# Kernel tuning notes

Hardware: AMD Instinct MI355X
Metric: run time of the kernel (lower is better)

Reference implementation:

```python
import jax, jax.numpy as jnp
import numpy as np

B, N, D = 4, 9216, 512
NH, L = 8, 64            # num_heads, num_landmarks
HD = D // NH             # head_dim = 64
MLP = 4 * D              # mlp_ratio 4.0


def setup_inputs() -> dict:
    key = jax.random.key(0)
    ks = jax.random.split(key, 32)
    w = lambda k, shape: jax.random.normal(k, shape, jnp.float32) * 0.02
    return {
        'x': jax.random.normal(ks[0], (B, N, D), jnp.float32),
        # PPEG depthwise convs (groups=dim -> kernel (D,1,kh,kw))
        'conv1_w': w(ks[1], (D, 1, 3, 3)), 'conv1_b': w(ks[2], (D,)),
        'conv2_w': w(ks[3], (D, 1, 5, 5)), 'conv2_b': w(ks[4], (D,)),
        'conv3_w': w(ks[5], (D, 1, 7, 7)), 'conv3_b': w(ks[6], (D,)),
        'ppeg_g': jnp.ones((D,), jnp.float32), 'ppeg_b': jnp.zeros((D,), jnp.float32),
        'norm1_g': jnp.ones((D,), jnp.float32), 'norm1_b': jnp.zeros((D,), jnp.float32),
        'norm2_g': jnp.ones((D,), jnp.float32), 'norm2_b': jnp.zeros((D,), jnp.float32),
        # Nystrom attention projections (torch Linear: y = x @ W.T + b)
        'qkv_w': w(ks[7], (3 * D, D)), 'qkv_b': w(ks[8], (3 * D,)),
        'proj_w': w(ks[9], (D, D)), 'proj_b': w(ks[10], (D,)),
        # MLP
        'mlp_w1': w(ks[11], (MLP, D)), 'mlp_b1': w(ks[12], (MLP,)),
        'mlp_w2': w(ks[13], (D, MLP)), 'mlp_b2': w(ks[14], (D,)),
    }


def _layernorm(x, g, b):
    m = jnp.mean(x, axis=-1, keepdims=True)
    v = jnp.mean(jnp.square(x - m), axis=-1, keepdims=True)
    return (x - m) * jax.lax.rsqrt(v + 1e-5) * g + b


def _dwconv(x2d, w, b, pad):
    # x2d: (B, D, H, W); depthwise conv, groups = D
    y = jax.lax.conv_general_dilated(
        x2d, w, window_strides=(1, 1), padding=((pad, pad), (pad, pad)),
        feature_group_count=w.shape[0],
        dimension_numbers=('NCHW', 'OIHW', 'NCHW'))
    return y + b[None, :, None, None]


def _forward(x, conv1_w, conv1_b, conv2_w, conv2_b, conv3_w, conv3_b,
             ppeg_g, ppeg_b, norm1_g, norm1_b, norm2_g, norm2_b,
             qkv_w, qkv_b, proj_w, proj_b, mlp_w1, mlp_b1, mlp_w2, mlp_b2):
    Bx, Nx, Dx = x.shape
    # ---- PPEG ----
    H = int(np.sqrt(Nx)); W = (Nx + H - 1) // H
    x2d = x.reshape(Bx, H, W, Dx).transpose(0, 3, 1, 2)  # b d h w
    pos = (_dwconv(x2d, conv1_w, conv1_b, 1)
           + _dwconv(x2d, conv2_w, conv2_b, 2)
           + _dwconv(x2d, conv3_w, conv3_b, 3))
    pos = pos.transpose(0, 2, 3, 1).reshape(Bx, Nx, Dx)
    x = _layernorm(x + pos, ppeg_g, ppeg_b)
    # ---- Nystrom attention ----
    xn = _layernorm(x, norm1_g, norm1_b)
    qkv = xn @ qkv_w.T + qkv_b                      # (B, N, 3D)
    qkv = qkv.reshape(Bx, Nx, 3, NH, HD).transpose(2, 0, 3, 1, 4)
    q, k, v = qkv[0], qkv[1], qkv[2]                # (B, H, N, hd)
    scale = HD ** -0.5
    idx = np.linspace(0, Nx - 1, L).astype(np.int64)  # landmark indices (static)
    kl, ql = k[:, :, idx], q[:, :, idx]             # (B, H, L, hd)
    k1 = jax.nn.softmax(jnp.einsum('bhnd,bhld->bhnl', q, kl) * scale, axis=-1)
    k2 = jax.nn.softmax(jnp.einsum('bhld,bhmd->bhlm', ql, kl) * scale, axis=-1)
    k3 = jax.nn.softmax(jnp.einsum('bhld,bhnd->bhln', ql, k) * scale, axis=-1)
    k2_inv = jnp.linalg.pinv(k2 + 1e-6 * jnp.eye(L, dtype=x.dtype))
    # (k1 @ k2_inv @ k3) @ v, right-associated to avoid the NxN intermediate
    out = k1 @ (k2_inv @ (k3 @ v))                  # (B, H, N, hd)
    out = out.transpose(0, 2, 1, 3).reshape(Bx, Nx, Dx)
    out = out @ proj_w.T + proj_b
    x = x + out
    # ---- MLP ----
    xn2 = _layernorm(x, norm2_g, norm2_b)
    h = jax.nn.gelu(xn2 @ mlp_w1.T + mlp_b1, approximate=False)
    x = x + (h @ mlp_w2.T + mlp_b2)
    return x


def reference(x, conv1_w, conv1_b, conv2_w, conv2_b, conv3_w, conv3_b,
              ppeg_g, ppeg_b, norm1_g, norm1_b, norm2_g, norm2_b,
              qkv_w, qkv_b, proj_w, proj_b, mlp_w1, mlp_b1, mlp_w2, mlp_b2):
    return _forward(x, conv1_w, conv1_b, conv2_w, conv2_b, conv3_w, conv3_b,
                    ppeg_g, ppeg_b, norm1_g, norm1_b, norm2_g, norm2_b,
                    qkv_w, qkv_b, proj_w, proj_b, mlp_w1, mlp_b1, mlp_w2, mlp_b2)
```

## Files before the change

kernel.cpp:

```cpp
#include <hip/hip_runtime.h>

typedef unsigned int u32;
typedef short bf16x8 __attribute__((ext_vector_type(8)));
typedef float f32x4 __attribute__((ext_vector_type(4)));
typedef u32 __attribute__((address_space(1))) u32g;
typedef u32 __attribute__((address_space(3))) u32l;

#define B_  4
#define N_  9216
#define D_  512
#define NH_ 8
#define HD_ 64
#define L_  64
#define HH_ 96
#define MT_ 36864
#define SCALE_ 0.125f
#define NS_ 4

__device__ __forceinline__ float bf2f(unsigned short u) {
    union { u32 i; float f; } c; c.i = ((u32)u) << 16; return c.f;
}
__device__ __forceinline__ unsigned short f2bf(float f) {
    u32 x = __float_as_uint(f);
    return (unsigned short)((x + 0x7fffu + ((x >> 16) & 1u)) >> 16);
}
__device__ __forceinline__ int lm_idx(int l){ return (l * 9215) / 63; }
__device__ __forceinline__ u32 pk2(float a, float b){ return (u32)f2bf(a) | ((u32)f2bf(b) << 16); }

#define PJW_N  262144
#define MLPW_N 1048576
__global__ __launch_bounds__(256)
void prep_weights(const float* __restrict__ pjw,
                  const float* __restrict__ w1, const float* __restrict__ w2,
                  unsigned short* __restrict__ pwh, unsigned short* __restrict__ pwl,
                  unsigned short* __restrict__ w1b, unsigned short* __restrict__ w2b)
{
    const int total = PJW_N + MLPW_N + MLPW_N;
    for (int i = blockIdx.x * 256 + threadIdx.x; i < total; i += gridDim.x * 256) {
        if (i < PJW_N) {
            float v = pjw[i]; unsigned short h = f2bf(v);
            pwh[i] = h; pwl[i] = f2bf(v - bf2f(h));
        } else if (i < PJW_N + MLPW_N) {
            int j = i - PJW_N;
            w1b[j] = f2bf(w1[j]);
        } else {
            int j = i - PJW_N - MLPW_N;
            w2b[j] = f2bf(w2[j]);
        }
    }
}

__global__ __launch_bounds__(512)
void ppeg_ln_kernel(const float* __restrict__ x,
                    const float* __restrict__ c1w, const float* __restrict__ c1b,
                    const float* __restrict__ c2w, const float* __restrict__ c2b,
                    const float* __restrict__ c3w, const float* __restrict__ c3b,
                    const float* __restrict__ pg, const float* __restrict__ pb,
                    float* __restrict__ x1, float* __restrict__ stats)
{
    const int b = blockIdx.x / HH_;
    const int h = blockIdx.x % HH_;
    const int d = threadIdx.x;
    const int tid = threadIdx.x;

    float wtap[49];
    #pragma unroll
    for (int i = 0; i < 49; ++i) wtap[i] = c3w[d * 49 + i];
    #pragma unroll
    for (int ky = 0; ky < 5; ++ky)
        #pragma unroll
        for (int kx = 0; kx < 5; ++kx)
            wtap[(ky + 1) * 7 + (kx + 1)] += c2w[d * 25 + ky * 5 + kx];
    #pragma unroll
    for (int ky = 0; ky < 3; ++ky)
        #pragma unroll
        for (int kx = 0; kx < 3; ++kx)
            wtap[(ky + 2) * 7 + (kx + 2)] += c1w[d * 9 + ky * 3 + kx];

    const float bsum = c1b[d] + c2b[d] + c3b[d];
    const float gpv = pg[d], bpv = pb[d];

    __shared__ float red[2][8];

    for (int w = 0; w < HH_; ++w) {
        float pos = bsum;
        float xc = 0.f;
        #pragma unroll
        for (int dy = -3; dy <= 3; ++dy) {
            int hh = h + dy;
            if (hh < 0 || hh >= HH_) continue;
            #pragma unroll
            for (int dx = -3; dx <= 3; ++dx) {
                int ww = w + dx;
                if (ww < 0 || ww >= HH_) continue;
                float xv = x[(size_t)(b * N_ + hh * HH_ + ww) * D_ + d];
                pos += xv * wtap[(dy + 3) * 7 + (dx + 3)];
                if (dy == 0 && dx == 0) xc = xv;
            }
        }
        float s = xc + pos;

        float sv = s, sq = s * s;
        #pragma unroll
        for (int o = 32; o > 0; o >>= 1) { sv += __shfl_down(sv, o); sq += __shfl_down(sq, o); }
        if ((tid & 63) == 0) { red[0][tid >> 6] = sv; red[1][tid >> 6] = sq; }
        __syncthreads();
        float tot = 0.f, totq = 0.f;
        #pragma unroll
        for (int i = 0; i < 8; ++i) { tot += red[0][i]; totq += red[1][i]; }
        __syncthreads();
        float mean = tot * (1.f / 512.f);
        float var  = totq * (1.f / 512.f) - mean * mean;
        float x1v = (s - mean) * rsqrtf(var + 1e-5f) * gpv + bpv;

        float sv2 = x1v, sq2 = x1v * x1v;
        #pragma unroll
        for (int o = 32; o > 0; o >>= 1) { sv2 += __shfl_down(sv2, o); sq2 += __shfl_down(sq2, o); }
        if ((tid & 63) == 0) { red[0][tid >> 6] = sv2; red[1][tid >> 6] = sq2; }
        __syncthreads();
        float tot2 = 0.f, totq2 = 0.f;
        #pragma unroll
        for (int i = 0; i < 8; ++i) { tot2 += red[0][i]; totq2 += red[1][i]; }
        __syncthreads();
        float m2 = tot2 * (1.f / 512.f);
        float v2 = totq2 * (1.f / 512.f) - m2 * m2;

        size_t row = (size_t)(b * N_ + h * HH_ + w);
        x1[row * D_ + d] = x1v;
        if (tid == 0) {
            stats[row * 2 + 0] = m2;
            stats[row * 2 + 1] = rsqrtf(v2 + 1e-5f);
        }
    }
}

__global__ __launch_bounds__(256)
void gemm_f32_qk(const float* __restrict__ X1, const float* __restrict__ stats,
                 const float* __restrict__ g1, const float* __restrict__ b1,
                 const float* __restrict__ qkvw, const float* __restrict__ qkvb,
                 float* __restrict__ qb, float* __restrict__ kb)
{
    __shared__ float xnS[128][33];
    __shared__ float wS[128][33];
    const int tid = threadIdx.x;
    const int n0 = blockIdx.x * 128;
    const int m0 = blockIdx.y * 128;
    const int tm = tid >> 4, tn = tid & 15;

    float acc[8][8];
    #pragma unroll
    for (int i = 0; i < 8; ++i)
        #pragma unroll
        for (int j = 0; j < 8; ++j) acc[i][j] = 0.f;

    for (int k0 = 0; k0 < 512; k0 += 32) {
        #pragma unroll
        for (int e = 0; e < 16; ++e) {
            int i = tid + 256 * e;
            int row = i >> 5, kk = i & 31;
            float xv = X1[(size_t)(m0 + row) * 512 + k0 + kk];
            float mean = stats[(m0 + row) * 2], rs = stats[(m0 + row) * 2 + 1];
            xnS[row][kk] = (xv - mean) * rs * g1[k0 + kk] + b1[k0 + kk];
            wS[row][kk] = qkvw[(size_t)(n0 + row) * 512 + k0 + kk];
        }
        __syncthreads();
        for (int kk = 0; kk < 32; ++kk) {
            float a_[8], b_[8];
            #pragma unroll
            for (int i = 0; i < 8; ++i) a_[i] = xnS[tm * 8 + i][kk];
            #pragma unroll
            for (int j = 0; j < 8; ++j) b_[j] = wS[tn + 16 * j][kk];
            #pragma unroll
            for (int i = 0; i < 8; ++i)
                #pragma unroll
                for (int j = 0; j < 8; ++j) acc[i][j] += a_[i] * b_[j];
        }
        __syncthreads();
    }
    #pragma unroll
    for (int i = 0; i < 8; ++i) {
        #pragma unroll
        for (int j = 0; j < 8; ++j) {
            int gm = m0 + tm * 8 + i;
            int gc = n0 + tn + 16 * j;
            int b = gm / N_, n = gm - b * N_;
            float v = acc[i][j] + qkvb[gc];
            if (gc < 512) {
                qb[(((size_t)b * NH_ + (gc >> 6)) * N_ + n) * HD_ + (gc & 63)] = v;
            } else {
                kb[(((size_t)b * NH_ + ((gc >> 6) - 8)) * N_ + n) * HD_ + (gc & 63)] = v;
            }
        }
    }
}

__global__ __launch_bounds__(256)
void extract_lm(const float* __restrict__ q, const float* __restrict__ k,
                float* __restrict__ qlf, float* __restrict__ klf,
                double* __restrict__ ql64, double* __restrict__ kl64)
{
    const int bh = blockIdx.x, tid = threadIdx.x;
    const int b = bh >> 3, h = bh & 7;
    for (int i = tid; i < 4096; i += 256) {
        int l = i >> 6, d = i & 63;
        size_t src = (((size_t)b * NH_ + h) * N_ + lm_idx(l)) * HD_ + d;
        float qv = q[src], kv = k[src];
        size_t dst = (size_t)bh * 4096 + i;
        qlf[dst] = qv; klf[dst] = kv;
        ql64[dst] = (double)qv; kl64[dst] = (double)kv;
    }
}

__global__ __launch_bounds__(256)
void k2pinv_kernel(const double* __restrict__ ql64, const double* __restrict__ kl64,
                   double* __restrict__ k2inv)
{
    const int bh = blockIdx.x;
    const int tid = threadIdx.x;
    const int lane = tid & 63, wv = tid >> 6;
    __shared__ double A[64][65];
    __shared__ double G[64][65];
    __shared__ double V[64][65];
    __shared__ double cS[32], sS[32], wS[64];
    __shared__ int pS[32], qS[32];
    __shared__ double lmaxS;

    for (int i = tid; i < 4096; i += 256) {
        int l = i >> 6, m = i & 63;
        const double* qp = ql64 + (size_t)bh * 4096 + l * 64;
        const double* kp = kl64 + (size_t)bh * 4096 + m * 64;
        double s = 0.0;
        for (int d = 0; d < 64; ++d) s += qp[d] * kp[d];
        A[l][m] = s * 0.125;
    }
    __syncthreads();
    if (tid < 64) {
        double mx = -1e300;
        for (int j = 0; j < 64; ++j) mx = fmax(mx, A[tid][j]);
        double sm = 0.0;
        for (int j = 0; j < 64; ++j) { double e = exp(A[tid][j] - mx); A[tid][j] = e; sm += e; }
        double inv = 1.0 / sm;
        for (int j = 0; j < 64; ++j) A[tid][j] *= inv;
        A[tid][tid] += 1e-6;
    }
    __syncthreads();
    for (int e = tid; e < 4096; e += 256) {
        int i = e >> 6, j = e & 63;
        double s = 0.0;
        for (int l = 0; l < 64; ++l) s += A[l][i] * A[l][j];
        G[i][j] = s;
        V[i][j] = (i == j) ? 1.0 : 0.0;
    }
    __syncthreads();
    for (int sweep = 0; sweep < 8; ++sweep) {
        for (int r = 0; r < 63; ++r) {
            if (tid < 32) {
                int p, q;
                if (tid == 0) { p = 63; q = r; }
                else { p = (r + tid) % 63; q = (r - tid + 63) % 63; }
                double app = G[p][p], aqq = G[q][q], apq = G[p][q];
                double c = 1.0, s = 0.0;
                if (fabs(apq) > 1e-200) {
                    double tau = (aqq - app) / (2.0 * apq);
                    double tt = ((tau >= 0.0) ? 1.0 : -1.0) / (fabs(tau) + sqrt(1.0 + tau * tau));
                    c = 1.0 / sqrt(1.0 + tt * tt);
                    s = tt * c;
                }
                pS[tid] = p; qS[tid] = q; cS[tid] = c; sS[tid] = s;
            }
            __syncthreads();
            int pA[8], qA[8];
            double cA[8], sA[8];
            #pragma unroll
            for (int t = 0; t < 8; ++t) {
                int pr = wv * 8 + t;
                pA[t] = pS[pr]; qA[t] = qS[pr]; cA[t] = cS[pr]; sA[t] = sS[pr];
            }
            {
                double gp[8], gq[8];
                #pragma unroll
                for (int t = 0; t < 8; ++t) { gp[t] = G[pA[t]][lane]; gq[t] = G[qA[t]][lane]; }
                #pragma unroll
                for (int t = 0; t < 8; ++t) {
                    G[pA[t]][lane] = cA[t] * gp[t] - sA[t] * gq[t];
                    G[qA[t]][lane] = sA[t] * gp[t] + cA[t] * gq[t];
                }
            }
            __syncthreads();
            {
                double gp[8], gq[8], vp[8], vq[8];
                #pragma unroll
                for (int t = 0; t < 8; ++t) { gp[t] = G[lane][pA[t]]; gq[t] = G[lane][qA[t]]; }
                #pragma unroll
                for (int t = 0; t < 8; ++t) { vp[t] = V[lane][pA[t]]; vq[t] = V[lane][qA[t]]; }
                #pragma unroll
                for (int t = 0; t < 8; ++t) {
                    G[lane][pA[t]] = cA[t] * gp[t] - sA[t] * gq[t];
                    G[lane][qA[t]] = sA[t] * gp[t] + cA[t] * gq[t];
                }
                #pragma unroll
                for (int t = 0; t < 8; ++t) {
                    V[lane][pA[t]] = cA[t] * vp[t] - sA[t] * vq[t];
                    V[lane][qA[t]] = sA[t] * vp[t] + cA[t] * vq[t];
                }
            }
            __syncthreads();
        }
    }
    if (tid == 0) {
        double lm = 0.0;
        for (int j = 0; j < 64; ++j) lm = fmax(lm, G[j][j]);
        lmaxS = lm;
    }
    __syncthreads();
    if (tid < 64) {
        const double rc = 7.62939453125e-5;
        double cut = rc * rc * lmaxS;
        double l = G[tid][tid];
        wS[tid] = (l > cut) ? (1.0 / l) : 0.0;
    }
    __syncthreads();
    for (int e = tid; e < 4096; e += 256) {
        int i = e >> 6, j = e & 63;
        double s = 0.0;
        for (int m = 0; m < 64; ++m) s += V[i][m] * wS[m] * V[j][m];
        G[i][j] = s;
    }
    __syncthreads();
    for (int e = tid; e < 4096; e += 256) {
        int i = e >> 6, j = e & 63;
        double s = 0.0;
        for (int m = 0; m < 64; ++m) s += G[i][m] * A[j][m];
        k2inv[(size_t)bh * 4096 + e] = s;
    }
}

__global__ __launch_bounds__(256)
void s3_u_kernel(const float* __restrict__ qlf, const float* __restrict__ k,
                 const float* __restrict__ X1, const float* __restrict__ stats,
                 const float* __restrict__ g1, const float* __restrict__ b1,
                 float* __restrict__ Up, float* __restrict__ sp)
{
    const int s = blockIdx.x;
    const int bh = blockIdx.y;
    const int dq = blockIdx.z;
    const int tid = threadIdx.x;
    const int b = bh >> 3;
    __shared__ float qlS[64][68];
    __shared__ float kS[16][68];
    __shared__ float S[64][17];
    __shared__ float xnS[16][132];
    __shared__ float gS[128], bS[128];
    const size_t kbase = (size_t)bh * N_ * HD_;
    const int f0 = dq * 128;

    for (int i = tid; i < 4096; i += 256) qlS[i >> 6][i & 63] = qlf[(size_t)bh * 4096 + i];
    if (tid < 128) { gS[tid] = g1[f0 + tid]; bS[tid] = b1[f0 + tid]; }

    const int lp = tid >> 3;
    const int fq = tid & 7;
    f32x4 acc0[4], acc1[4];
    #pragma unroll
    for (int j = 0; j < 4; ++j) { acc0[j] = (f32x4){0,0,0,0}; acc1[j] = (f32x4){0,0,0,0}; }
    float sacc0 = 0.f, sacc1 = 0.f;

    const int nchunks = (N_ / NS_) / 16;
    for (int c = 0; c < nchunks; ++c) {
        const int n0 = s * (N_ / NS_) + c * 16;
        __syncthreads();
        {
            int i = tid * 4;
            int n = i >> 6, d = i & 63;
            float4 v = *(const float4*)(k + kbase + (size_t)(n0 + n) * HD_ + d);
            kS[n][d + 0] = v.x; kS[n][d + 1] = v.y; kS[n][d + 2] = v.z; kS[n][d + 3] = v.w;
        }
        {
            int i = tid * 8;
            int r = i >> 7, fl = i & 127;
            int gm = b * N_ + n0 + r;
            float mean = stats[gm * 2], rs = stats[gm * 2 + 1];
            const float* xp = X1 + (size_t)gm * 512 + f0 + fl;
            float4 v0 = *(const float4*)(xp);
            float4 v1 = *(const float4*)(xp + 4);
            float xv[8] = {v0.x, v0.y, v0.z, v0.w, v1.x, v1.y, v1.z, v1.w};
            #pragma unroll
            for (int e = 0; e < 8; ++e) {
                int f = fl + e;
                float val = (xv[e] - mean) * rs * gS[f] + bS[f];
                int g = f >> 2;
                int slot = ((g & 3) << 3) | (g >> 2);
                xnS[r][slot * 4 + (f & 3)] = val;
            }
        }
        __syncthreads();
        {
            const int n = tid & 15;
            const int l0 = (tid >> 4) << 2;
            const f32x4* kr4 = (const f32x4*)&kS[n][0];
            const f32x4* q0 = (const f32x4*)&qlS[l0 + 0][0];
            const f32x4* q1 = (const f32x4*)&qlS[l0 + 1][0];
            const f32x4* q2 = (const f32x4*)&qlS[l0 + 2][0];
            const f32x4* q3 = (const f32x4*)&qlS[l0 + 3][0];
            float s0 = 0.f, s1 = 0.f, s2 = 0.f, s3 = 0.f;
            #pragma unroll
            for (int d4 = 0; d4 < 16; ++d4) {
                f32x4 kv = kr4[d4];
                f32x4 a0 = q0[d4], a1 = q1[d4], a2 = q2[d4], a3 = q3[d4];
                s0 += a0.x * kv.x + a0.y * kv.y + a0.z * kv.z + a0.w * kv.w;
                s1 += a1.x * kv.x + a1.y * kv.y + a1.z * kv.z + a1.w * kv.w;
                s2 += a2.x * kv.x + a2.y * kv.y + a2.z * kv.z + a2.w * kv.w;
                s3 += a3.x * kv.x + a3.y * kv.y + a3.z * kv.z + a3.w * kv.w;
            }
            S[l0 + 0][n] = expf(s0 * SCALE_);
            S[l0 + 1][n] = expf(s1 * SCALE_);
            S[l0 + 2][n] = expf(s2 * SCALE_);
            S[l0 + 3][n] = expf(s3 * SCALE_);
        }
        __syncthreads();
        for (int n = 0; n < 16; ++n) {
            float p0 = S[2 * lp + 0][n];
            float p1 = S[2 * lp + 1][n];
            const f32x4* xr = (const f32x4*)&xnS[n][0];
            #pragma unroll
            for (int j = 0; j < 4; ++j) {
                f32x4 xv = xr[fq + 8 * j];
                acc0[j].x += p0 * xv.x; acc0[j].y += p0 * xv.y;
                acc0[j].z += p0 * xv.z; acc0[j].w += p0 * xv.w;
                acc1[j].x += p1 * xv.x; acc1[j].y += p1 * xv.y;
                acc1[j].z += p1 * xv.z; acc1[j].w += p1 * xv.w;
            }
            if (dq == 0 && fq == 0) { sacc0 += p0; sacc1 += p1; }
        }
    }
    {
        size_t ubase = (((size_t)bh * NS_ + s) * 64) * 512;
        float4* u0 = (float4*)(Up + ubase + (size_t)(2 * lp + 0) * 512 + f0 + fq * 16);
        float4* u1 = (float4*)(Up + ubase + (size_t)(2 * lp + 1) * 512 + f0 + fq * 16);
        #pragma unroll
        for (int j = 0; j < 4; ++j) {
            u0[j] = (float4){acc0[j].x, acc0[j].y, acc0[j].z, acc0[j].w};
            u1[j] = (float4){acc1[j].x, acc1[j].y, acc1[j].z, acc1[j].w};
        }
    }
    if (dq == 0 && fq == 0) {
        sp[((size_t)bh * NS_ + s) * 64 + 2 * lp + 0] = sacc0;
        sp[((size_t)bh * NS_ + s) * 64 + 2 * lp + 1] = sacc1;
    }
}

__global__ __launch_bounds__(256)
void combine_u_kernel(const float* __restrict__ Up, const float* __restrict__ sp,
                      float* __restrict__ Un)
{
    const int bh = blockIdx.x, tid = threadIdx.x;
    __shared__ float dro[64];
    if (tid < 64) {
        float d = 0.f;
        for (int s = 0; s < NS_; ++s) d += sp[((size_t)bh * NS_ + s) * 64 + tid];
        dro[tid] = d;
    }
    __syncthreads();
    for (int i = tid; i < 64 * 512; i += 256) {
        int l = i >> 9;
        float a = 0.f;
        for (int s = 0; s < NS_; ++s) a += Up[(((size_t)bh * NS_ + s) * 64) * 512 + i];
        Un[(size_t)bh * 64 * 512 + i] = a / dro[l];
    }
}

__global__ __launch_bounds__(256)
void tn_kernel(const float* __restrict__ Un, const float* __restrict__ qkvw,
               const float* __restrict__ qkvb, float* __restrict__ Tn)
{
    const int bh = blockIdx.x, tid = threadIdx.x;
    const int h = bh & 7;
    const int l = tid >> 2, d0 = (tid & 3) * 16;
    const float* un = Un + (size_t)bh * 64 * 512 + l * 512;
    for (int j = 0; j < 16; ++j) {
        int d = d0 + j;
        const float* wv = qkvw + (size_t)(1024 + h * 64 + d) * 512;
        float t = 0.f;
        for (int f = 0; f < 512; ++f) t += un[f] * wv[f];
        Tn[(size_t)bh * 4096 + l * 64 + d] = t + qkvb[1024 + h * 64 + d];
    }
}

__global__ __launch_bounds__(256)
void combine_b_kernel(const float* __restrict__ Tn, const double* __restrict__ k2inv,
                      float* __restrict__ W2)
{
    const int bh = blockIdx.x, tid = threadIdx.x;
    __shared__ float Tl[64][64];
    for (int i = tid; i < 4096; i += 256) Tl[i >> 6][i & 63] = Tn[(size_t)bh * 4096 + i];
    __syncthreads();
    const int l = tid >> 2, d0 = (tid & 3) * 16;
    float o[16];
    #pragma unroll
    for (int j = 0; j < 16; ++j) o[j] = 0.f;
    const double* kr = k2inv + (size_t)bh * 4096 + l * 64;
    for (int j2 = 0; j2 < 64; ++j2) {
        float a = (float)kr[j2];
        const float* tr = &Tl[j2][d0];
        #pragma unroll
        for (int j = 0; j < 16; ++j) o[j] += a * tr[j];
    }
    float* wp = W2 + (size_t)bh * 4096 + l * 64 + d0;
    #pragma unroll
    for (int j = 0; j < 16; ++j) wp[j] = o[j];
}

__global__ __launch_bounds__(256)
void k1pv_kernel(const float* __restrict__ q, const float* __restrict__ klf,
                 const float* __restrict__ W2,
                 unsigned short* __restrict__ atth, unsigned short* __restrict__ attl)
{
    const int nc = blockIdx.x;
    const int bh = blockIdx.y;
    const int tid = threadIdx.x;
    __shared__ float klS[64][64];
    __shared__ float W2S[64][64];
    const size_t base = (size_t)bh * N_ * HD_;
    for (int i = tid; i < 4096; i += 256) {
        klS[i >> 6][i & 63] = klf[(size_t)bh * 4096 + i];
        W2S[i >> 6][i & 63] = W2[(size_t)bh * 4096 + i];
    }
    __syncthreads();
    const int n = nc * 256 + tid;
    float qf[64];
    const float4* qr = (const float4*)(q + base + (size_t)n * HD_);
    #pragma unroll
    for (int j = 0; j < 16; ++j) { float4 u = qr[j]; qf[j*4]=u.x; qf[j*4+1]=u.y; qf[j*4+2]=u.z; qf[j*4+3]=u.w; }
    float s[64];
    #pragma unroll
    for (int l = 0; l < 64; ++l) {
        const f32x4* kl4 = (const f32x4*)&klS[l][0];
        float t = 0.f;
        #pragma unroll
        for (int d4 = 0; d4 < 16; ++d4) {
            f32x4 w4 = kl4[d4];
            t += w4.x * qf[d4*4] + w4.y * qf[d4*4+1] + w4.z * qf[d4*4+2] + w4.w * qf[d4*4+3];
        }
        s[l] = t * SCALE_;
    }
    float mx = -1e30f;
    #pragma unroll
    for (int l = 0; l < 64; ++l) mx = fmaxf(mx, s[l]);
    float sum = 0.f;
    #pragma unroll
    for (int l = 0; l < 64; ++l) { s[l] = expf(s[l] - mx); sum += s[l]; }
    float inv = 1.f / sum;
    float acc[64];
    #pragma unroll
    for (int d2 = 0; d2 < 64; ++d2) acc[d2] = 0.f;
    #pragma unroll
    for (int l = 0; l < 64; ++l) {
        float p = s[l] * inv;
        const f32x4* w4p = (const f32x4*)&W2S[l][0];
        #pragma unroll
        for (int d4 = 0; d4 < 16; ++d4) {
            f32x4 w4 = w4p[d4];
            acc[d4*4+0] += p * w4.x; acc[d4*4+1] += p * w4.y;
            acc[d4*4+2] += p * w4.z; acc[d4*4+3] += p * w4.w;
        }
    }
    unsigned short* oh = atth + base + (size_t)n * HD_;
    unsigned short* ol = attl + base + (size_t)n * HD_;
    #pragma unroll
    for (int j = 0; j < 8; ++j) {
        float hv[8], lv[8];
        #pragma unroll
        for (int e = 0; e < 8; ++e) {
            float a = acc[j * 8 + e];
            unsigned short hb = f2bf(a);
            hv[e] = bf2f(hb);
            lv[e] = a - hv[e];
        }
        uint4 uh, ul;
        uh.x = pk2(hv[0], hv[1]); uh.y = pk2(hv[2], hv[3]);
        uh.z = pk2(hv[4], hv[5]); uh.w = pk2(hv[6], hv[7]);
        ul.x = pk2(lv[0], lv[1]); ul.y = pk2(lv[2], lv[3]);
        ul.z = pk2(lv[4], lv[5]); ul.w = pk2(lv[6], lv[7]);
        ((uint4*)oh)[j] = uh;
        ((uint4*)ol)[j] = ul;
    }
}

__global__ __launch_bounds__(256)
void gemm_proj(const unsigned short* __restrict__ Aa, const unsigned short* __restrict__ Ab,
               const unsigned short* __restrict__ Wh, const unsigned short* __restrict__ Wl,
               const float* __restrict__ bias, float* __restrict__ fo0)
{
    __shared__ __align__(16) char AsH[8192];
    __shared__ __align__(16) char AsL[8192];
    __shared__ __align__(16) char BsH[4096];
    __shared__ __align__(16) char BsL[4096];
    const int tid = threadIdx.x;
    const int wv = tid >> 6, lane = tid & 63;
    const int wm = wv >> 1, wn = wv & 1;
    const int n0 = blockIdx.x * 64;
    const int m0 = blockIdx.y * 128;

    f32x4 acc[4][2];
    #pragma unroll
    for (int i = 0; i < 4; ++i)
        #pragma unroll
        for (int j = 0; j < 2; ++j) acc[i][j] = (f32x4){0.f, 0.f, 0.f, 0.f};

    for (int k0 = 0; k0 < 512; k0 += 32) {
        {
            int row = wv * 16 + (lane >> 2);
            int sl = lane & 3;
            int kk = k0 + ((sl ^ (row & 3)) << 3);
            const unsigned short* s0 = Wh + (size_t)(n0 + row) * 512 + kk;
            __builtin_amdgcn_global_load_lds((const u32g*)s0, (u32l*)(BsH + wv * 1024), 16, 0, 0);
            const unsigned short* s1 = Wl + (size_t)(n0 + row) * 512 + kk;
            __builtin_amdgcn_global_load_lds((const u32g*)s1, (u32l*)(BsL + wv * 1024), 16, 0, 0);
        }
        #pragma unroll
        for (int t = 0; t < 2; ++t) {
            int row = wv * 32 + t * 16 + (lane >> 2);
            int sl = lane & 3;
            int kk = k0 + ((sl ^ (row & 3)) << 3);
            int m = m0 + row;
            int b = m / N_; int n = m - b * N_; int hh = kk >> 6; int dd = kk & 63;
            size_t adr = (((size_t)b * NH_ + hh) * N_ + n) * HD_ + dd;
            __builtin_amdgcn_global_load_lds((const u32g*)(Aa + adr),
                                             (u32l*)(AsH + wv * 2048 + t * 1024), 16, 0, 0);
            __builtin_amdgcn_global_load_lds((const u32g*)(Ab + adr),
                                             (u32l*)(AsL + wv * 2048 + t * 1024), 16, 0, 0);
        }
        __syncthreads();
        bf16x8 afh[4], afl[4], bfh[2], bfl[2];
        #pragma unroll
        for (int mf = 0; mf < 4; ++mf) {
            int r = wm * 64 + mf * 16 + (lane & 15);
            int ps = (lane >> 4) ^ (r & 3);
            afh[mf] = *(const bf16x8*)(AsH + r * 64 + ps * 16);
            afl[mf] = *(const bf16x8*)(AsL + r * 64 + ps * 16);
        }
        #pragma unroll
        for (int nf = 0; nf < 2; ++nf) {
            int r = wn * 32 + nf * 16 + (lane & 15);
            int ps = (lane >> 4) ^ (r & 3);
            bfh[nf] = *(const bf16x8*)(BsH + r * 64 + ps * 16);
            bfl[nf] = *(const bf16x8*)(BsL + r * 64 + ps * 16);
        }
        #pragma unroll
        for (int mf = 0; mf < 4; ++mf)
            #pragma unroll
            for (int nf = 0; nf < 2; ++nf) {
                acc[mf][nf] = __builtin_amdgcn_mfma_f32_16x16x32_bf16(afh[mf], bfh[nf], acc[mf][nf], 0, 0, 0);
                acc[mf][nf] = __builtin_amdgcn_mfma_f32_16x16x32_bf16(afh[mf], bfl[nf], acc[mf][nf], 0, 0, 0);
                acc[mf][nf] = __builtin_amdgcn_mfma_f32_16x16x32_bf16(afl[mf], bfh[nf], acc[mf][nf], 0, 0, 0);
            }
        __syncthreads();
    }

    const int lc = lane & 15, lr4 = (lane >> 4) * 4;
    float bcol[2];
    #pragma unroll
    for (int nf = 0; nf < 2; ++nf)
        bcol[nf] = bias[n0 + wn * 32 + nf * 16 + lc];

    #pragma unroll
    for (int mf = 0; mf < 4; ++mf) {
        #pragma unroll
        for (int nf = 0; nf < 2; ++nf) {
            #pragma unroll
            for (int i = 0; i < 4; ++i) {
                int gm = m0 + wm * 64 + mf * 16 + lr4 + i;
                int gn = n0 + wn * 32 + nf * 16 + lc;
                fo0[(size_t)gm * 512 + gn] = acc[mf][nf][i] + bcol[nf];
            }
        }
    }
}

__global__ __launch_bounds__(256)
void resid_ln_kernel(const float* __restrict__ x1, float* __restrict__ pjo_x2,
                     const float* __restrict__ g, const float* __restrict__ bb,
                     unsigned short* __restrict__ xn2h)
{
    const int row = blockIdx.x, tid = threadIdx.x;
    const size_t base = (size_t)row * D_;
    float a0 = x1[base + tid]       + pjo_x2[base + tid];
    float a1 = x1[base + 256 + tid] + pjo_x2[base + 256 + tid];
    __shared__ float red[2][4];
    float sv = a0 + a1, sq = a0 * a0 + a1 * a1;
    #pragma unroll
    for (int o = 32; o > 0; o >>= 1) { sv += __shfl_down(sv, o); sq += __shfl_down(sq, o); }
    if ((tid & 63) == 0) { red[0][tid >> 6] = sv; red[1][tid >> 6] = sq; }
    __syncthreads();
    float tot = 0.f, totq = 0.f;
    #pragma unroll
    for (int i = 0; i < 4; ++i) { tot += red[0][i]; totq += red[1][i]; }
    float mean = tot * (1.f / 512.f);
    float var  = totq * (1.f / 512.f) - mean * mean;
    float rs = rsqrtf(var + 1e-5f);
    float o0 = (a0 - mean) * rs * g[tid]       + bb[tid];
    float o1 = (a1 - mean) * rs * g[256 + tid] + bb[256 + tid];
    pjo_x2[base + tid] = a0;
    pjo_x2[base + 256 + tid] = a1;
    xn2h[base + tid] = f2bf(o0);
    xn2h[base + 256 + tid] = f2bf(o1);
}

#define E_GELU 0
#define E_ACC 1
#define E_FIN 2

template<int KLEN, int ALDA, int WLDA, int EPI, int OSTR>
__global__ __launch_bounds__(256)
void gemm_plain(const unsigned short* __restrict__ Aa,
                const unsigned short* __restrict__ Wh,
                int wrow0, int wcol0,
                const float* __restrict__ bias, int bias0,
                unsigned short* __restrict__ bo0, float* __restrict__ fo0,
                const unsigned short* __restrict__ accb, const float* __restrict__ resid)
{
    __shared__ __align__(16) char As[16384];
    __shared__ __align__(16) char Bs[16384];
    const int tid = threadIdx.x;
    const int wv = tid >> 6, lane = tid & 63;
    const int wm = wv >> 1, wn = wv & 1;
    const int n0 = blockIdx.x * 128;
    const int m0 = blockIdx.y * 128;
    const int rl = lane >> 3, sl = lane & 7;

    f32x4 acc[4][4];
    #pragma unroll
    for (int i = 0; i < 4; ++i)
        #pragma unroll
        for (int j = 0; j < 4; ++j) acc[i][j] = (f32x4){0.f, 0.f, 0.f, 0.f};

    for (int k0 = 0; k0 < KLEN; k0 += 64) {
        #pragma unroll
        for (int t = 0; t < 4; ++t) {
            int row = wv * 32 + t * 8 + rl;
            int slot = sl ^ (row & 7);
            const unsigned short* srcW = Wh + (size_t)(wrow0 + n0 + row) * WLDA + wcol0 + k0 + slot * 8;
            __builtin_amdgcn_global_load_lds((const u32g*)srcW, (u32l*)(Bs + wv * 4096 + t * 1024), 16, 0, 0);
            const unsigned short* srcA = Aa + (size_t)(m0 + row) * ALDA + k0 + slot * 8;
            __builtin_amdgcn_global_load_lds((const u32g*)srcA, (u32l*)(As + wv * 4096 + t * 1024), 16, 0, 0);
        }
        __syncthreads();
        #pragma unroll
        for (int ks = 0; ks < 2; ++ks) {
            bf16x8 af[4], bfr[4];
            #pragma unroll
            for (int mf = 0; mf < 4; ++mf) {
                int r = wm * 64 + mf * 16 + (lane & 15);
                int ps = (ks * 4 + (lane >> 4)) ^ (r & 7);
                af[mf] = *(const bf16x8*)(As + r * 128 + ps * 16);
            }
            #pragma unroll
            for (int nf = 0; nf < 4; ++nf) {
                int r = wn * 64 + nf * 16 + (lane & 15);
                int ps = (ks * 4 + (lane >> 4)) ^ (r & 7);
                bfr[nf] = *(const bf16x8*)(Bs + r * 128 + ps * 16);
            }
            #pragma unroll
            for (int mf = 0; mf < 4; ++mf)
                #pragma unroll
                for (int nf = 0; nf < 4; ++nf)
                    acc[mf][nf] = __builtin_amdgcn_mfma_f32_16x16x32_bf16(af[mf], bfr[nf], acc[mf][nf], 0, 0, 0);
        }
        __syncthreads();
    }

    const int lc = lane & 15, lr4 = (lane >> 4) * 4;
    float bcol[4];
    #pragma unroll
    for (int nf = 0; nf < 4; ++nf)
        bcol[nf] = bias ? bias[bias0 + n0 + wn * 64 + nf * 16 + lc] : 0.f;

    #pragma unroll
    for (int mf = 0; mf < 4; ++mf) {
        #pragma unroll
        for (int nf = 0; nf < 4; ++nf) {
            #pragma unroll
            for (int i = 0; i < 4; ++i) {
                int gm = m0 + wm * 64 + mf * 16 + lr4 + i;
                int gn = n0 + wn * 64 + nf * 16 + lc;
                float val = acc[mf][nf][i] + bcol[nf];
                if (EPI == E_GELU) {
                    float g = 0.5f * val * (1.f + erff(val * 0.70710678118f));
                    bo0[(size_t)gm * OSTR + gn] = f2bf(g);
                } else if (EPI == E_ACC) {
                    bo0[(size_t)gm * OSTR + gn] = f2bf(val);
                } else {
                    fo0[(size_t)gm * 512 + gn] = val + bf2f(accb[(size_t)gm * 512 + gn])
                                               + resid[(size_t)gm * 512 + gn];
                }
            }
        }
    }
}

extern "C" void kernel_launch(void* const* d_in, const int* in_sizes, int n_in,
                              void* d_out, int out_size, void* d_ws, size_t ws_size,
                              hipStream_t stream) {
    const float* x    = (const float*)d_in[0];
    const float* c1w  = (const float*)d_in[1];
    const float* c1b  = (const float*)d_in[2];
    const float* c2w  = (const float*)d_in[3];
    const float* c2b  = (const float*)d_in[4];
    const float* c3w  = (const float*)d_in[5];
    const float* c3b  = (const float*)d_in[6];
    const float* pg   = (const float*)d_in[7];
    const float* pb   = (const float*)d_in[8];
    const float* n1g  = (const float*)d_in[9];
    const float* n1b  = (const float*)d_in[10];
    const float* n2g  = (const float*)d_in[11];
    const float* n2b  = (const float*)d_in[12];
    const float* qkvw = (const float*)d_in[13];
    const float* qkvb = (const float*)d_in[14];
    const float* pjw  = (const float*)d_in[15];
    const float* pjb  = (const float*)d_in[16];
    const float* w1   = (const float*)d_in[17];
    const float* b1   = (const float*)d_in[18];
    const float* w2m  = (const float*)d_in[19];
    const float* b2m  = (const float*)d_in[20];

    char* ws = (char*)d_ws;
    char* RA = ws;
    char* RB = ws + 75497472;
    char* RC = ws + 150994944;
    char* R3 = ws + 226492416;
    unsigned short* pwh  = (unsigned short*)(R3 + 0);
    unsigned short* pwl  = (unsigned short*)(R3 + 524288);
    unsigned short* w1b  = (unsigned short*)(R3 + 1048576);
    unsigned short* w2b  = (unsigned short*)(R3 + 3145728);
    float*  stats = (float*)(R3 + 5242880);
    float*  qlf   = (float*)(R3 + 5537792);
    float*  klf   = (float*)(R3 + 6062080);
    double* ql64  = (double*)(R3 + 6586368);
    double* kl64  = (double*)(R3 + 7634944);
    double* k2i   = (double*)(R3 + 8683520);
    float*  W2    = (float*)(R3 + 9732096);
    float*  Tn    = (float*)(R3 + 10256384);
    float*  sp    = (float*)(R3 + 10780672);
    float*  Up    = (float*)(R3 + 10813440);
    float*  Un    = (float*)(R3 + 27590656);

    float* x1 = (float*)RA;
    float* kb = (float*)RB;
    float* qb = (float*)RC;
    unsigned short* atth = (unsigned short*)RB;
    unsigned short* attl = (unsigned short*)(RB + 37748736);
    float* pjo = (float*)RC;
    unsigned short* xn2  = (unsigned short*)RB;
    unsigned short* accb = (unsigned short*)(RB + 37748736);
    unsigned short* hbuf = (unsigned short*)RA;

    prep_weights<<<1024, 256, 0, stream>>>(pjw, w1, w2m, pwh, pwl, w1b, w2b);
    ppeg_ln_kernel<<<B_ * HH_, 512, 0, stream>>>(x, c1w, c1b, c2w, c2b, c3w, c3b,
                                                 pg, pb, x1, stats);
    gemm_f32_qk<<<dim3(8, 288), 256, 0, stream>>>(x1, stats, n1g, n1b, qkvw, qkvb, qb, kb);
    extract_lm<<<32, 256, 0, stream>>>(qb, kb, qlf, klf, ql64, kl64);
    k2pinv_kernel<<<32, 256, 0, stream>>>(ql64, kl64, k2i);
    s3_u_kernel<<<dim3(NS_, 32, 4), 256, 0, stream>>>(qlf, kb, x1, stats, n1g, n1b, Up, sp);
    combine_u_kernel<<<32, 256, 0, stream>>>(Up, sp, Un);
    tn_kernel<<<32, 256, 0, stream>>>(Un, qkvw, qkvb, Tn);
    combine_b_kernel<<<32, 256, 0, stream>>>(Tn, k2i, W2);
    k1pv_kernel<<<dim3(36, 32), 256, 0, stream>>>(qb, klf, W2, atth, attl);
    gemm_proj<<<dim3(8, 288), 256, 0, stream>>>(atth, attl, pwh, pwl, pjb, pjo);
    resid_ln_kernel<<<MT_, 256, 0, stream>>>(x1, pjo, n2g, n2b, xn2);
    gemm_plain<512, 512, 512, E_GELU, 1024><<<dim3(8, 288), 256, 0, stream>>>(
        xn2, w1b, 0, 0, b1, 0, hbuf, nullptr, nullptr, nullptr);
    gemm_plain<1024, 1024, 2048, E_ACC, 512><<<dim3(4, 288), 256, 0, stream>>>(
        hbuf, w2b, 0, 0, nullptr, 0, accb, nullptr, nullptr, nullptr);
    gemm_plain<512, 512, 512, E_GELU, 1024><<<dim3(8, 288), 256, 0, stream>>>(
        xn2, w1b, 1024, 0, b1, 1024, hbuf, nullptr, nullptr, nullptr);
    gemm_plain<1024, 1024, 2048, E_FIN, 512><<<dim3(4, 288), 256, 0, stream>>>(
        hbuf, w2b, 0, 1024, b2m, 0, nullptr, (float*)d_out, accb, pjo);
}
```

Measured before the change: 4.549 ms.

## Split PPEG rows across more blocks and reuse a sliding 7x7 register window

The PPEG+LayerNorm kernel previously ran one block per image row (384 blocks), each looping over 96 columns and reloading all 49 taps from global memory per output. It now launches 8 blocks per row, each handling 12 columns, and keeps a 7x7 register window that slides horizontally so each step loads only one new column of 7 values. This raises parallelism on a GPU with many CUs and cuts redundant global loads, at the cost of more registers per thread and a 6-column halo reload per block.

```diff
diff --git a/kernel.cpp b/kernel.cpp
--- a/kernel.cpp
+++ b/kernel.cpp
@@ -58,8 +58,10 @@
                     const float* __restrict__ pg, const float* __restrict__ pb,
                     float* __restrict__ x1, float* __restrict__ stats)
 {
-    const int b = blockIdx.x / HH_;
-    const int h = blockIdx.x % HH_;
+    const int bh = blockIdx.y;
+    const int b = bh / HH_;
+    const int h = bh % HH_;
+    const int w0 = blockIdx.x * 12;
     const int d = threadIdx.x;
     const int tid = threadIdx.x;
 
@@ -82,22 +84,38 @@
 
     __shared__ float red[2][8];
 
-    for (int w = 0; w < HH_; ++w) {
+    float win[7][7];
+    #pragma unroll
+    for (int r = 0; r < 7; ++r) {
+        int hh = h + r - 3;
+        bool hok = (hh >= 0 && hh < HH_);
+        #pragma unroll
+        for (int j = 0; j < 6; ++j) {
+            int ww = w0 - 3 + j;
+            win[r][j] = (hok && ww >= 0 && ww < HH_)
+                      ? x[(size_t)(b * N_ + hh * HH_ + ww) * D_ + d] : 0.f;
+        }
+    }
+
+    for (int wi = 0; wi < 12; ++wi) {
+        const int w = w0 + wi;
+        {
+            int ww = w + 3;
+            bool wok = (ww < HH_);
+            #pragma unroll
+            for (int r = 0; r < 7; ++r) {
+                int hh = h + r - 3;
+                win[r][6] = (wok && hh >= 0 && hh < HH_)
+                          ? x[(size_t)(b * N_ + hh * HH_ + ww) * D_ + d] : 0.f;
+            }
+        }
         float pos = bsum;
-        float xc = 0.f;
-        #pragma unroll
-        for (int dy = -3; dy <= 3; ++dy) {
-            int hh = h + dy;
-            if (hh < 0 || hh >= HH_) continue;
-            #pragma unroll
-            for (int dx = -3; dx <= 3; ++dx) {
-                int ww = w + dx;
-                if (ww < 0 || ww >= HH_) continue;
-                float xv = x[(size_t)(b * N_ + hh * HH_ + ww) * D_ + d];
-                pos += xv * wtap[(dy + 3) * 7 + (dx + 3)];
-                if (dy == 0 && dx == 0) xc = xv;
-            }
-        }
+        #pragma unroll
+        for (int r = 0; r < 7; ++r)
+            #pragma unroll
+            for (int j = 0; j < 7; ++j)
+                pos += win[r][j] * wtap[r * 7 + j];
+        float xc = win[3][3];
         float s = xc + pos;
 
         float sv = s, sq = s * s;
@@ -131,6 +149,11 @@
             stats[row * 2 + 0] = m2;
             stats[row * 2 + 1] = rsqrtf(v2 + 1e-5f);
         }
+        #pragma unroll
+        for (int r = 0; r < 7; ++r)
+            #pragma unroll
+            for (int j = 0; j < 6; ++j)
+                win[r][j] = win[r][j + 1];
     }
 }
 
@@ -854,8 +877,8 @@
     unsigned short* hbuf = (unsigned short*)RA;
 
     prep_weights<<<1024, 256, 0, stream>>>(pjw, w1, w2m, pwh, pwl, w1b, w2b);
-    ppeg_ln_kernel<<<B_ * HH_, 512, 0, stream>>>(x, c1w, c1b, c2w, c2b, c3w, c3b,
-                                                 pg, pb, x1, stats);
+    ppeg_ln_kernel<<<dim3(8, B_ * HH_), 512, 0, stream>>>(x, c1w, c1b, c2w, c2b, c3w, c3b,
+                                                          pg, pb, x1, stats);
     gemm_f32_qk<<<dim3(8, 288), 256, 0, stream>>>(x1, stats, n1g, n1b, qkvw, qkvb, qb, kb);
     extract_lm<<<32, 256, 0, stream>>>(qb, kb, qlf, klf, ql64, kl64);
     k2pinv_kernel<<<32, 256, 0, stream>>>(ql64, kl64, k2i);
```

New measurement: 3.845 ms. 1.18x faster.
